# Optimization experiments

Measured on AMD Instinct MI355X. Metric: run time of the kernel, lower is better.

The kernel has to match this reference:

```python
import jax, jax.numpy as jnp
import numpy as np

N, E, G = 100000, 800000, 1000
N_IN, NHID, HEADS, NOUT = 128, 32, 4, 768
HC = NHID * HEADS


def setup_inputs() -> dict:
    key = jax.random.key(0)
    ks = jax.random.split(key, 12)
    s = 1.0 / np.sqrt(N_IN)
    inp = {
        "x": jax.random.normal(ks[0], (N, N_IN), jnp.float32),
        "edge_index": jax.random.randint(ks[1], (2, E), 0, N, jnp.int64),
        "batch": jnp.sort(jax.random.randint(ks[2], (N,), 0, G, jnp.int64)),
        "Wq": jax.random.uniform(ks[3], (N_IN, HC), jnp.float32, -s, s),
        "bq": jnp.zeros((HC,), jnp.float32),
        "Wk": jax.random.uniform(ks[4], (N_IN, HC), jnp.float32, -s, s),
        "bk": jnp.zeros((HC,), jnp.float32),
        "Wv": jax.random.uniform(ks[5], (N_IN, HC), jnp.float32, -s, s),
        "bv": jnp.zeros((HC,), jnp.float32),
        "Wskip": jax.random.uniform(ks[6], (N_IN, HC), jnp.float32, -s, s),
        "bskip": jnp.zeros((HC,), jnp.float32),
        "Wbeta": jax.random.uniform(ks[7], (3 * HC, 1), jnp.float32, -1.0 / np.sqrt(3 * HC), 1.0 / np.sqrt(3 * HC)),
        "W2": jax.random.uniform(ks[8], (HC, NOUT), jnp.float32, -1.0 / np.sqrt(HC), 1.0 / np.sqrt(HC)),
        "b2": jnp.zeros((NOUT,), jnp.float32),
    }
    return inp


def _transformer_net(x, edge_index, batch, Wq, bq, Wk, bk, Wv, bv, Wskip, bskip, Wbeta, W2, b2):
    src, dst = edge_index[0], edge_index[1]  # messages src -> dst
    q = (x @ Wq + bq).reshape(N, HEADS, NHID)
    k = (x @ Wk + bk).reshape(N, HEADS, NHID)
    v = (x @ Wv + bv).reshape(N, HEADS, NHID)
    # edge-wise attention logits [E, H]
    alpha = jnp.einsum('ehc,ehc->eh', q[dst], k[src]) / np.sqrt(NHID)
    # segment softmax over incoming edges of each destination node
    m = jax.ops.segment_max(alpha, dst, num_segments=N)  # [N, H]
    e = jnp.exp(alpha - m[dst])
    denom = jax.ops.segment_sum(e, dst, num_segments=N)  # [N, H]
    attn = e / (denom[dst] + 1e-16)  # [E, H]
    msg = v[src] * attn[..., None]  # [E, H, C]
    out = jax.ops.segment_sum(msg, dst, num_segments=N).reshape(N, HC)
    # beta gating (root skip)
    skip = x @ Wskip + bskip  # [N, HC]
    beta = jax.nn.sigmoid(jnp.concatenate([out, skip, out - skip], axis=-1) @ Wbeta)  # [N, 1]
    out = beta * skip + (1.0 - beta) * out
    # LeakyReLU (default slope 0.01)
    out = jnp.where(out >= 0, out, 0.01 * out)
    # global mean pool per graph
    sums = jax.ops.segment_sum(out, batch, num_segments=G)  # [G, HC]
    cnts = jax.ops.segment_sum(jnp.ones((N,), out.dtype), batch, num_segments=G)
    pooled = sums / jnp.maximum(cnts, 1.0)[:, None]
    return pooled @ W2 + b2  # [G, NOUT]


def reference(x, edge_index, batch, Wq, bq, Wk, bk, Wv, bv, Wskip, bskip, Wbeta, W2, b2):
    return _transformer_net(x, edge_index, batch, Wq, bq, Wk, bk, Wv, bv, Wskip, bskip, Wbeta, W2, b2)
```

## Files before the change

### kernel.cpp

```cpp
#include <hip/hip_runtime.h>
#include <hip/hip_bf16.h>
#include <hip/hip_fp8.h>
#include <math.h>

#define NIN 128
#define HC 128
#define NOUT 768
#define KVSTRIDE 384

typedef __attribute__((ext_vector_type(8))) short bf16x8;
typedef __attribute__((ext_vector_type(4))) float f32x4;
typedef __attribute__((ext_vector_type(4))) unsigned short ushort4v;
typedef __attribute__((ext_vector_type(8))) unsigned short ushort8v;

__device__ __forceinline__ unsigned short f2bf(float f) {
    __hip_bfloat16 h = __float2bfloat16(f);
    return *(unsigned short*)&h;
}

__device__ __forceinline__ float bfe(ushort8v u, int j) {
    return __uint_as_float(((unsigned int)u[j]) << 16);
}

__device__ __forceinline__ float f8tof(unsigned char b) {
    __hip_fp8_e4m3 h; h.__x = b; return (float)h;
}
__device__ __forceinline__ unsigned char ftof8(float f) {
    __hip_fp8_e4m3 h(f); return h.__x;
}

__global__ __launch_bounds__(256) void prep_hist(
    const float* __restrict__ Wq, const float* __restrict__ Wk,
    const float* __restrict__ Wv, const float* __restrict__ Wsk,
    unsigned short* __restrict__ Wtb,
    const int* __restrict__ ei, int* __restrict__ cnt, int E)
{
    if (blockIdx.x < 4) {
        const float* W = (blockIdx.x == 0) ? Wq : (blockIdx.x == 1) ? Wk
                       : (blockIdx.x == 2) ? Wv : Wsk;
        unsigned short* out = Wtb + (size_t)blockIdx.x * 128 * 128;
        const int t = threadIdx.x;
        for (int s = 0; s < 16; ++s) {
            const int f = t + s * 256;
            const int k = f >> 5;
            const int n = (f & 31) * 4;
            float4 w4 = *(const float4*)(W + (size_t)k * 128 + n);
            out[(size_t)(n    ) * 128 + k] = f2bf(w4.x);
            out[(size_t)(n + 1) * 128 + k] = f2bf(w4.y);
            out[(size_t)(n + 2) * 128 + k] = f2bf(w4.z);
            out[(size_t)(n + 3) * 128 + k] = f2bf(w4.w);
        }
    } else {
        const int e = (blockIdx.x - 4) * 256 + threadIdx.x;
        if (e < E) atomicAdd(cnt + ei[E + e], 1);
    }
}

__global__ __launch_bounds__(1024) void scan_part(
    const int* __restrict__ cnt, int* __restrict__ start,
    int* __restrict__ bsum, int N)
{
    __shared__ int wsum[16];
    const int tid = threadIdx.x;
    const int lane = tid & 63;
    const int w = tid >> 6;
    const int i = blockIdx.x * 1024 + tid;
    const int v = (i < N) ? cnt[i] : 0;
    int xv = v;
    #pragma unroll
    for (int off = 1; off < 64; off <<= 1) {
        const int y = __shfl_up(xv, off, 64);
        if (lane >= off) xv += y;
    }
    if (lane == 63) wsum[w] = xv;
    __syncthreads();
    if (tid < 16) {
        int y = wsum[tid];
        #pragma unroll
        for (int off = 1; off < 16; off <<= 1) {
            const int z = __shfl_up(y, off, 64);
            if (tid >= off) y += z;
        }
        wsum[tid] = y;
    }
    __syncthreads();
    const int excl = (w > 0 ? wsum[w - 1] : 0) + xv - v;
    if (i < N) start[i] = excl;
    if (tid == 1023) bsum[blockIdx.x] = wsum[15];
}

__global__ __launch_bounds__(256) void scan_add(
    int* __restrict__ start, int* __restrict__ cursor,
    const int* __restrict__ bsum, int N, int NB)
{
    __shared__ int pref;
    const int i = blockIdx.x * 256 + threadIdx.x;
    const int chunk = (blockIdx.x * 256) >> 10;
    if (threadIdx.x == 0) {
        int s = 0;
        for (int b = 0; b < chunk; ++b) s += bsum[b];
        pref = s;
    }
    __syncthreads();
    if (i < N) {
        const int s = start[i] + pref;
        start[i] = s;
        cursor[i] = s;
    }
}

__global__ __launch_bounds__(256, 4) void gemm_scatter(
    const float* __restrict__ x, const unsigned short* __restrict__ Wtb,
    const float* __restrict__ bk, const float* __restrict__ bv,
    unsigned char* __restrict__ kvb, int N,
    const int* __restrict__ ei, int* __restrict__ cursor,
    int* __restrict__ csr_src, int E, int nGemm)
{
    __shared__ unsigned short At[128][136];

    if ((int)blockIdx.x >= nGemm) {
        const int e = (blockIdx.x - nGemm) * 256 + threadIdx.x;
        if (e < E) {
            const int d = ei[E + e];
            const int pos = atomicAdd(cursor + d, 1);
            csr_src[pos] = ei[e];
        }
        return;
    }

    const int tid = threadIdx.x;
    const int lane = tid & 63;
    const int wave = tid >> 6;
    const int rowBase = blockIdx.x * 128;
    const bool full = (rowBase + 128 <= N);

    #pragma unroll
    for (int s = 0; s < 16; ++s) {
        const int f = tid + s * 256;
        const int r = f >> 5;
        const int cl = (f & 31) * 4;
        const int gr = rowBase + r;
        float4 a4 = make_float4(0.f, 0.f, 0.f, 0.f);
        if (full || gr < N) a4 = *(const float4*)(x + (size_t)gr * 128 + cl);
        ushort4v u;
        u.x = f2bf(a4.x); u.y = f2bf(a4.y); u.z = f2bf(a4.z); u.w = f2bf(a4.w);
        *(ushort4v*)&At[r][cl] = u;
    }
    __syncthreads();

    bf16x8 afr[2][4];
    #pragma unroll
    for (int m = 0; m < 2; ++m)
        #pragma unroll
        for (int kk = 0; kk < 4; ++kk)
            afr[m][kk] = *(bf16x8*)&At[wave * 32 + m * 16 + (lane & 15)]
                                    [kk * 32 + (lane >> 4) * 8];

    const int colb = lane & 15;
    const int kofs = (lane >> 4) * 8;
    const int g4   = (lane >> 4) * 4;

    #pragma unroll
    for (int w2 = 0; w2 < 2; ++w2) {
        const unsigned short* Wp = Wtb + (size_t)(1 + w2) * 128 * 128;
        const float* bias = (w2 == 0) ? bk : bv;

        f32x4 acc[2][8];
        #pragma unroll
        for (int m = 0; m < 2; ++m)
            #pragma unroll
            for (int nr = 0; nr < 8; ++nr)
                acc[m][nr] = (f32x4){0.f, 0.f, 0.f, 0.f};

        #pragma unroll
        for (int nr = 0; nr < 8; ++nr) {
            bf16x8 bfr[4];
            #pragma unroll
            for (int kk = 0; kk < 4; ++kk)
                bfr[kk] = *(const bf16x8*)(Wp + (size_t)(nr * 16 + colb) * 128
                                               + kk * 32 + kofs);
            #pragma unroll
            for (int kk = 0; kk < 4; ++kk) {
                #pragma unroll
                for (int m = 0; m < 2; ++m)
                    acc[m][nr] = __builtin_amdgcn_mfma_f32_16x16x32_bf16(
                        bfr[kk], afr[m][kk], acc[m][nr], 0, 0, 0);
            }
        }

        #pragma unroll
        for (int m = 0; m < 2; ++m) {
            const int xrow = rowBase + wave * 32 + m * 16 + (lane & 15);
            if (full || xrow < N) {
                unsigned char* row = kvb + (size_t)xrow * KVSTRIDE;
                #pragma unroll
                for (int nr = 0; nr < 8; ++nr) {
                    const int colb4 = nr * 16 + g4;
                    const float4 b4 = *(const float4*)(bias + colb4);
                    if (w2 == 0) {
                        unsigned int p = (unsigned int)ftof8(acc[m][nr][0] + b4.x)
                                       | ((unsigned int)ftof8(acc[m][nr][1] + b4.y) << 8)
                                       | ((unsigned int)ftof8(acc[m][nr][2] + b4.z) << 16)
                                       | ((unsigned int)ftof8(acc[m][nr][3] + b4.w) << 24);
                        *(unsigned int*)(row + colb4) = p;
                    } else {
                        ushort4v pk;
                        pk.x = f2bf(acc[m][nr][0] + b4.x);
                        pk.y = f2bf(acc[m][nr][1] + b4.y);
                        pk.z = f2bf(acc[m][nr][2] + b4.z);
                        pk.w = f2bf(acc[m][nr][3] + b4.w);
                        *(ushort4v*)(row + 128 + 2 * colb4) = pk;
                    }
                }
            }
        }
    }
}

__global__ __launch_bounds__(512) void node_aggr_fused(
    const float* __restrict__ x, const unsigned short* __restrict__ Wtb,
    const float* __restrict__ bq, const float* __restrict__ bsk,
    const unsigned char* __restrict__ kvb,
    const int* __restrict__ start, const int* __restrict__ cnt,
    const int* __restrict__ csr_src, const float* __restrict__ Wbeta,
    __hip_bfloat16* __restrict__ gout, int N)
{
    __shared__ unsigned short At[32][136];
    __shared__ unsigned short q_l[32][136];
    __shared__ unsigned short sk_l[32][136];

    const int tid = threadIdx.x;
    const int lane = tid & 63;
    const int wave = tid >> 6;
    const int n0 = blockIdx.x * 32;

    const int g  = lane >> 4;
    const int t  = lane & 15;
    const int ch = t * 8;
    const int r  = wave * 4 + g;
    const int n  = n0 + r;
    const bool nok = (n < N);
    int s0v = 0, cntv = 0;
    if (nok) { s0v = start[n]; cntv = cnt[n]; }

    #pragma unroll
    for (int s = 0; s < 2; ++s) {
        const int f = tid + s * 512;
        const int rr = f >> 5;
        const int cl = (f & 31) * 4;
        const int gr = n0 + rr;
        float4 a4 = make_float4(0.f, 0.f, 0.f, 0.f);
        if (gr < N) a4 = *(const float4*)(x + (size_t)gr * 128 + cl);
        ushort4v u;
        u.x = f2bf(a4.x); u.y = f2bf(a4.y); u.z = f2bf(a4.z); u.w = f2bf(a4.w);
        *(ushort4v*)&At[rr][cl] = u;
    }
    __syncthreads();

    {
        const int mh = wave >> 2;
        bf16x8 afr[4];
        #pragma unroll
        for (int kk = 0; kk < 4; ++kk)
            afr[kk] = *(bf16x8*)&At[mh * 16 + (lane & 15)][kk * 32 + (lane >> 4) * 8];
        const int colb = lane & 15;
        const int kofs = (lane >> 4) * 8;
        const int g4m  = (lane >> 4) * 4;
        const int rm   = mh * 16 + (lane & 15);

        f32x4 acc[2][2];
        #pragma unroll
        for (int a = 0; a < 2; ++a)
            #pragma unroll
            for (int b = 0; b < 2; ++b)
                acc[a][b] = (f32x4){0.f, 0.f, 0.f, 0.f};

        #pragma unroll
        for (int nr2 = 0; nr2 < 2; ++nr2) {
            const int nr = (wave & 3) * 2 + nr2;
            #pragma unroll
            for (int wsel = 0; wsel < 2; ++wsel) {
                const unsigned short* Wp = Wtb + (size_t)(wsel == 0 ? 0 : 3) * 128 * 128;
                bf16x8 bfr[4];
                #pragma unroll
                for (int kk = 0; kk < 4; ++kk)
                    bfr[kk] = *(const bf16x8*)(Wp + (size_t)(nr * 16 + colb) * 128
                                                   + kk * 32 + kofs);
                #pragma unroll
                for (int kk = 0; kk < 4; ++kk)
                    acc[wsel][nr2] = __builtin_amdgcn_mfma_f32_16x16x32_bf16(
                        bfr[kk], afr[kk], acc[wsel][nr2], 0, 0, 0);
            }
        }

        #pragma unroll
        for (int nr2 = 0; nr2 < 2; ++nr2) {
            const int col = ((wave & 3) * 2 + nr2) * 16 + g4m;
            ushort4v qp, sp;
            #pragma unroll
            for (int j = 0; j < 4; ++j) {
                qp[j] = f2bf(acc[0][nr2][j] + bq[col + j]);
                sp[j] = f2bf(acc[1][nr2][j] + bsk[col + j]);
            }
            *(ushort4v*)&q_l[rm][col]  = qp;
            *(ushort4v*)&sk_l[rm][col] = sp;
        }
    }
    __syncthreads();

    const float scale = 0.17677669529663687f;

    float qv[8];
    {
        const ushort8v q8 = *(const ushort8v*)&q_l[r][ch];
        #pragma unroll
        for (int j = 0; j < 8; ++j) qv[j] = bfe(q8, j);
    }

    const int e1v = s0v + cntv;
    float den = 0.f;
    float acc[8];
    #pragma unroll
    for (int j = 0; j < 8; ++j) acc[j] = 0.f;

    for (int base = s0v; base < e1v; base += 16) {
        const int nblk = min(16, e1v - base);
        const int sidx = csr_src[base + min(t, nblk - 1)];
        int sa = __shfl(sidx, g * 16, 64);
        int sb = __shfl(sidx, g * 16 + min(1, nblk - 1), 64);
        const unsigned char* rowa = kvb + (size_t)sa * KVSTRIDE;
        const unsigned char* rowb = kvb + (size_t)sb * KVSTRIDE;
        uint2 ka = *(const uint2*)(rowa + ch);
        ushort8v va = *(const ushort8v*)(rowa + 128 + 2 * ch);
        uint2 kb = *(const uint2*)(rowb + ch);
        ushort8v vb = *(const ushort8v*)(rowb + 128 + 2 * ch);
        int j = 0;
        for (; j + 1 < nblk; j += 2) {
            const int sna = __shfl(sidx, g * 16 + min(j + 2, nblk - 1), 64);
            const int snb = __shfl(sidx, g * 16 + min(j + 3, nblk - 1), 64);
            const unsigned char* rna = kvb + (size_t)sna * KVSTRIDE;
            const unsigned char* rnb = kvb + (size_t)snb * KVSTRIDE;
            const uint2 kna = *(const uint2*)(rna + ch);
            const ushort8v vna = *(const ushort8v*)(rna + 128 + 2 * ch);
            const uint2 knb = *(const uint2*)(rnb + ch);
            const ushort8v vnb = *(const ushort8v*)(rnb + 128 + 2 * ch);
            float pa = 0.f, pb = 0.f;
            #pragma unroll
            for (int jj = 0; jj < 4; ++jj) {
                pa = fmaf(f8tof((ka.x >> (8 * jj)) & 0xff), qv[jj], pa);
                pa = fmaf(f8tof((ka.y >> (8 * jj)) & 0xff), qv[4 + jj], pa);
                pb = fmaf(f8tof((kb.x >> (8 * jj)) & 0xff), qv[jj], pb);
                pb = fmaf(f8tof((kb.y >> (8 * jj)) & 0xff), qv[4 + jj], pb);
            }
            pa += __shfl_xor(pa, 1, 64);
            pa += __shfl_xor(pa, 2, 64);
            pb += __shfl_xor(pb, 1, 64);
            pb += __shfl_xor(pb, 2, 64);
            const float exa = __expf(pa * scale);
            const float exb = __expf(pb * scale);
            den += exa + exb;
            #pragma unroll
            for (int jj = 0; jj < 8; ++jj)
                acc[jj] = fmaf(bfe(va, jj), exa, fmaf(bfe(vb, jj), exb, acc[jj]));
            ka = kna; va = vna; kb = knb; vb = vnb;
        }
        if (j < nblk) {
            float pa = 0.f;
            #pragma unroll
            for (int jj = 0; jj < 4; ++jj) {
                pa = fmaf(f8tof((ka.x >> (8 * jj)) & 0xff), qv[jj], pa);
                pa = fmaf(f8tof((ka.y >> (8 * jj)) & 0xff), qv[4 + jj], pa);
            }
            pa += __shfl_xor(pa, 1, 64);
            pa += __shfl_xor(pa, 2, 64);
            const float exa = __expf(pa * scale);
            den += exa;
            #pragma unroll
            for (int jj = 0; jj < 8; ++jj) acc[jj] = fmaf(bfe(va, jj), exa, acc[jj]);
        }
    }

    const float inv = 1.f / (den + 1e-16f);
    float o[8], sk[8];
    {
        const ushort8v s8 = *(const ushort8v*)&sk_l[r][ch];
        #pragma unroll
        for (int j = 0; j < 8; ++j) sk[j] = bfe(s8, j);
    }
    float part = 0.f;
    #pragma unroll
    for (int j = 0; j < 8; ++j) {
        o[j] = acc[j] * inv;
        part += o[j] * Wbeta[ch + j] + sk[j] * Wbeta[HC + ch + j]
              + (o[j] - sk[j]) * Wbeta[2 * HC + ch + j];
    }
    part += __shfl_xor(part, 1, 64);
    part += __shfl_xor(part, 2, 64);
    part += __shfl_xor(part, 4, 64);
    part += __shfl_xor(part, 8, 64);

    const float beta = 1.f / (1.f + __expf(-part));
    if (nok) {
        union { unsigned short h[8]; ushort8v v8; } pk;
        #pragma unroll
        for (int j = 0; j < 8; ++j) {
            float rv = beta * sk[j] + (1.f - beta) * o[j];
            rv = (rv >= 0.f) ? rv : 0.01f * rv;
            pk.h[j] = f2bf(rv);
        }
        *(ushort8v*)(gout + (size_t)n * HC + ch) = pk.v8;
    }
}

__global__ __launch_bounds__(256) void pool_final(
    const __hip_bfloat16* __restrict__ gout, const int* __restrict__ batch,
    const float* __restrict__ W2, const float* __restrict__ b2,
    float* __restrict__ out, int N, int G)
{
    const int g0 = blockIdx.x * 4;
    __shared__ float p[4][HC];
    const int wave = threadIdx.x >> 6;
    const int lane = threadIdx.x & 63;
    const int g = g0 + wave;
    if (g < G) {
        int lo = 0, hi = N;
        while (lo < hi) { const int m = (lo + hi) >> 1; if (batch[m] < g) lo = m + 1; else hi = m; }
        int lo2 = lo, hi2 = N;
        while (lo2 < hi2) { const int m = (lo2 + hi2) >> 1; if (batch[m] < g + 1) lo2 = m + 1; else hi2 = m; }
        float a0 = 0.f, a1 = 0.f;
        for (int r = lo; r < lo2; ++r) {
            const __hip_bfloat162 g2 = *(const __hip_bfloat162*)(gout + (size_t)r * HC + 2 * lane);
            a0 += __bfloat162float(g2.x);
            a1 += __bfloat162float(g2.y);
        }
        const float invc = 1.f / fmaxf((float)(lo2 - lo), 1.f);
        p[wave][2 * lane]     = a0 * invc;
        p[wave][2 * lane + 1] = a1 * invc;
    }
    __syncthreads();
    const int t = threadIdx.x;
    for (int j = t; j < NOUT; j += 256) {
        const float bj = b2[j];
        float a0 = bj, a1 = bj, a2 = bj, a3 = bj;
        #pragma unroll 4
        for (int c = 0; c < HC; ++c) {
            const float w = W2[(size_t)c * NOUT + j];
            a0 = fmaf(p[0][c], w, a0);
            a1 = fmaf(p[1][c], w, a1);
            a2 = fmaf(p[2][c], w, a2);
            a3 = fmaf(p[3][c], w, a3);
        }
        if (g0     < G) out[(size_t)(g0    ) * NOUT + j] = a0;
        if (g0 + 1 < G) out[(size_t)(g0 + 1) * NOUT + j] = a1;
        if (g0 + 2 < G) out[(size_t)(g0 + 2) * NOUT + j] = a2;
        if (g0 + 3 < G) out[(size_t)(g0 + 3) * NOUT + j] = a3;
    }
}

extern "C" void kernel_launch(void* const* d_in, const int* in_sizes, int n_in,
                              void* d_out, int out_size, void* d_ws, size_t ws_size,
                              hipStream_t stream) {
    const float* x     = (const float*)d_in[0];
    const int*   ei    = (const int*)d_in[1];
    const int*   batch = (const int*)d_in[2];
    const float* Wq  = (const float*)d_in[3];  const float* bq  = (const float*)d_in[4];
    const float* Wk  = (const float*)d_in[5];  const float* bk  = (const float*)d_in[6];
    const float* Wv  = (const float*)d_in[7];  const float* bv  = (const float*)d_in[8];
    const float* Wsk = (const float*)d_in[9];  const float* bsk = (const float*)d_in[10];
    const float* Wbeta = (const float*)d_in[11];
    const float* W2  = (const float*)d_in[12]; const float* b2  = (const float*)d_in[13];

    const int N = in_sizes[0] / NIN;
    const int E = in_sizes[1] / 2;
    const int G = out_size / NOUT;

    char* ws = (char*)d_ws;
    unsigned char* kvb = (unsigned char*)ws;
    char* p0 = ws + (size_t)N * KVSTRIDE;
    unsigned short* Wtb = (unsigned short*)p0;            p0 += 4 * 128 * 128 * sizeof(unsigned short);
    int* cnt    = (int*)p0;                               p0 += (size_t)N * sizeof(int);
    int* start  = (int*)p0;                               p0 += (size_t)N * sizeof(int);
    int* cursor = (int*)p0;                               p0 += (size_t)N * sizeof(int);
    int* bsum   = (int*)p0;                               p0 += 1024 * sizeof(int);
    int* csr    = (int*)p0;                               p0 += (size_t)E * sizeof(int);
    __hip_bfloat16* gout = (__hip_bfloat16*)p0;

    hipMemsetAsync(cnt, 0, (size_t)N * sizeof(int), stream);

    const int eb = (E + 255) / 256;
    const int NB = (N + 1023) / 1024;
    const int nGemm = (N + 127) / 128;

    prep_hist<<<4 + eb, 256, 0, stream>>>(Wq, Wk, Wv, Wsk, Wtb, ei, cnt, E);
    scan_part<<<NB, 1024, 0, stream>>>(cnt, start, bsum, N);
    scan_add<<<(N + 255) / 256, 256, 0, stream>>>(start, cursor, bsum, N, NB);
    gemm_scatter<<<nGemm + eb, 256, 0, stream>>>(x, Wtb, bk, bv, kvb, N,
                                                 ei, cursor, csr, E, nGemm);

    node_aggr_fused<<<(N + 31) / 32, 512, 0, stream>>>(x, Wtb, bq, bsk, kvb,
                                                       start, cnt, csr, Wbeta,
                                                       gout, N);

    pool_final<<<(G + 3) / 4, 256, 0, stream>>>(gout, batch, W2, b2,
                                                (float*)d_out, N, G);
}
```

Baseline: 266.5 us.

## Sort nodes by in-degree bucket to balance per-wave aggregation work

Builds a degree histogram in scan_add, scans it into bucket offsets in a new single-wave kernel, and counting-sorts node indices into a perm array inside extra gemm_scatter blocks. node_aggr_fused then processes nodes in perm order, so nodes handled by one wave have similar edge counts and lanes idle less on uneven degrees. It also adds a launch-bounds occupancy hint and a sched_barrier in the edge loop. The cost is an extra small kernel launch, atomics, the perm array, and scattered x reads and gout writes.

```diff
diff --git a/kernel.cpp b/kernel.cpp
--- a/kernel.cpp
+++ b/kernel.cpp
@@ -91,11 +91,14 @@
 
 __global__ __launch_bounds__(256) void scan_add(
     int* __restrict__ start, int* __restrict__ cursor,
-    const int* __restrict__ bsum, int N, int NB)
+    const int* __restrict__ bsum, const int* __restrict__ cnt,
+    int* __restrict__ bins, int N, int NB)
 {
     __shared__ int pref;
+    __shared__ int lbins[64];
     const int i = blockIdx.x * 256 + threadIdx.x;
     const int chunk = (blockIdx.x * 256) >> 10;
+    if (threadIdx.x < 64) lbins[threadIdx.x] = 0;
     if (threadIdx.x == 0) {
         int s = 0;
         for (int b = 0; b < chunk; ++b) s += bsum[b];
@@ -106,7 +109,25 @@
         const int s = start[i] + pref;
         start[i] = s;
         cursor[i] = s;
-    }
+        atomicAdd(&lbins[min(cnt[i], 63)], 1);
+    }
+    __syncthreads();
+    if (threadIdx.x < 64 && lbins[threadIdx.x])
+        atomicAdd(bins + threadIdx.x, lbins[threadIdx.x]);
+}
+
+__global__ __launch_bounds__(64) void bucket_scan(
+    const int* __restrict__ bins, int* __restrict__ bcur)
+{
+    const int t = threadIdx.x;
+    const int v = bins[t];
+    int xv = v;
+    #pragma unroll
+    for (int off = 1; off < 64; off <<= 1) {
+        const int y = __shfl_up(xv, off, 64);
+        if (t >= off) xv += y;
+    }
+    bcur[t] = xv - v;
 }
 
 __global__ __launch_bounds__(256, 4) void gemm_scatter(
@@ -114,9 +135,28 @@
     const float* __restrict__ bk, const float* __restrict__ bv,
     unsigned char* __restrict__ kvb, int N,
     const int* __restrict__ ei, int* __restrict__ cursor,
-    int* __restrict__ csr_src, int E, int nGemm)
+    int* __restrict__ csr_src, int E, int nGemm, int nScat,
+    const int* __restrict__ cnt, int* __restrict__ bcur, int* __restrict__ perm)
 {
     __shared__ unsigned short At[128][136];
+
+    if ((int)blockIdx.x >= nGemm + nScat) {
+        __shared__ int lh[64], lbase[64];
+        const int idx = (blockIdx.x - nGemm - nScat) * 256 + threadIdx.x;
+        if (threadIdx.x < 64) lh[threadIdx.x] = 0;
+        __syncthreads();
+        int d = 0, slot = 0;
+        if (idx < N) {
+            d = min(cnt[idx], 63);
+            slot = atomicAdd(&lh[d], 1);
+        }
+        __syncthreads();
+        if (threadIdx.x < 64 && lh[threadIdx.x])
+            lbase[threadIdx.x] = atomicAdd(bcur + threadIdx.x, lh[threadIdx.x]);
+        __syncthreads();
+        if (idx < N) perm[lbase[d] + slot] = idx;
+        return;
+    }
 
     if ((int)blockIdx.x >= nGemm) {
         const int e = (blockIdx.x - nGemm) * 256 + threadIdx.x;
@@ -217,12 +257,13 @@
     }
 }
 
-__global__ __launch_bounds__(512) void node_aggr_fused(
+__global__ __launch_bounds__(512, 4) void node_aggr_fused(
     const float* __restrict__ x, const unsigned short* __restrict__ Wtb,
     const float* __restrict__ bq, const float* __restrict__ bsk,
     const unsigned char* __restrict__ kvb,
     const int* __restrict__ start, const int* __restrict__ cnt,
     const int* __restrict__ csr_src, const float* __restrict__ Wbeta,
+    const int* __restrict__ perm,
     __hip_bfloat16* __restrict__ gout, int N)
 {
     __shared__ unsigned short At[32][136];
@@ -240,17 +281,21 @@
     const int r  = wave * 4 + g;
     const int n  = n0 + r;
     const bool nok = (n < N);
+    const int pn = nok ? perm[n] : 0;
     int s0v = 0, cntv = 0;
-    if (nok) { s0v = start[n]; cntv = cnt[n]; }
+    if (nok) { s0v = start[pn]; cntv = cnt[pn]; }
 
     #pragma unroll
     for (int s = 0; s < 2; ++s) {
         const int f = tid + s * 512;
         const int rr = f >> 5;
         const int cl = (f & 31) * 4;
-        const int gr = n0 + rr;
+        const int gn = n0 + rr;
         float4 a4 = make_float4(0.f, 0.f, 0.f, 0.f);
-        if (gr < N) a4 = *(const float4*)(x + (size_t)gr * 128 + cl);
+        if (gn < N) {
+            const int ps = perm[gn];
+            a4 = *(const float4*)(x + (size_t)ps * 128 + cl);
+        }
         ushort4v u;
         u.x = f2bf(a4.x); u.y = f2bf(a4.y); u.z = f2bf(a4.z); u.w = f2bf(a4.w);
         *(ushort4v*)&At[rr][cl] = u;
@@ -344,6 +389,7 @@
             const ushort8v vna = *(const ushort8v*)(rna + 128 + 2 * ch);
             const uint2 knb = *(const uint2*)(rnb + ch);
             const ushort8v vnb = *(const ushort8v*)(rnb + 128 + 2 * ch);
+            __builtin_amdgcn_sched_barrier(0);
             float pa = 0.f, pb = 0.f;
             #pragma unroll
             for (int jj = 0; jj < 4; ++jj) {
@@ -408,7 +454,7 @@
             rv = (rv >= 0.f) ? rv : 0.01f * rv;
             pk.h[j] = f2bf(rv);
         }
-        *(ushort8v*)(gout + (size_t)n * HC + ch) = pk.v8;
+        *(ushort8v*)(gout + (size_t)pn * HC + ch) = pk.v8;
     }
 }
 
@@ -479,27 +525,33 @@
     char* p0 = ws + (size_t)N * KVSTRIDE;
     unsigned short* Wtb = (unsigned short*)p0;            p0 += 4 * 128 * 128 * sizeof(unsigned short);
     int* cnt    = (int*)p0;                               p0 += (size_t)N * sizeof(int);
+    int* bins   = (int*)p0;                               p0 += 64 * sizeof(int);
+    int* bcur   = (int*)p0;                               p0 += 64 * sizeof(int);
     int* start  = (int*)p0;                               p0 += (size_t)N * sizeof(int);
     int* cursor = (int*)p0;                               p0 += (size_t)N * sizeof(int);
     int* bsum   = (int*)p0;                               p0 += 1024 * sizeof(int);
     int* csr    = (int*)p0;                               p0 += (size_t)E * sizeof(int);
+    int* perm   = (int*)p0;                               p0 += (size_t)N * sizeof(int);
     __hip_bfloat16* gout = (__hip_bfloat16*)p0;
 
-    hipMemsetAsync(cnt, 0, (size_t)N * sizeof(int), stream);
+    hipMemsetAsync(cnt, 0, ((size_t)N + 64) * sizeof(int), stream);
 
     const int eb = (E + 255) / 256;
     const int NB = (N + 1023) / 1024;
     const int nGemm = (N + 127) / 128;
+    const int nPerm = (N + 255) / 256;
 
     prep_hist<<<4 + eb, 256, 0, stream>>>(Wq, Wk, Wv, Wsk, Wtb, ei, cnt, E);
     scan_part<<<NB, 1024, 0, stream>>>(cnt, start, bsum, N);
-    scan_add<<<(N + 255) / 256, 256, 0, stream>>>(start, cursor, bsum, N, NB);
-    gemm_scatter<<<nGemm + eb, 256, 0, stream>>>(x, Wtb, bk, bv, kvb, N,
-                                                 ei, cursor, csr, E, nGemm);
+    scan_add<<<(N + 255) / 256, 256, 0, stream>>>(start, cursor, bsum, cnt, bins, N, NB);
+    bucket_scan<<<1, 64, 0, stream>>>(bins, bcur);
+    gemm_scatter<<<nGemm + eb + nPerm, 256, 0, stream>>>(x, Wtb, bk, bv, kvb, N,
+                                                         ei, cursor, csr, E,
+                                                         nGemm, eb, cnt, bcur, perm);
 
     node_aggr_fused<<<(N + 31) / 32, 512, 0, stream>>>(x, Wtb, bq, bsk, kvb,
                                                        start, cnt, csr, Wbeta,
-                                                       gout, N);
+                                                       perm, gout, N);
 
     pool_final<<<(G + 3) / 4, 256, 0, stream>>>(gout, batch, W2, b2,
                                                 (float*)d_out, N, G);
```

Result: slower. 285.3 us (+7.0%).
